# Kernel optimization log

Hardware: AMD Instinct MI355X
Metric: run time of the kernel (lower is better)

The kernel has to match this reference:

```python
import jax, jax.numpy as jnp
import numpy as np

B, L, D, N_HEADS = 4, 8192, 1024, 16
HD = D // N_HEADS
MASK_NEG = -1e10


def setup_inputs() -> dict:
    key = jax.random.key(0)
    ks = jax.random.split(key, 5)
    # xavier_normal std for square Dense: sqrt(2/(fan_in+fan_out))
    std = (2.0 / (D + D)) ** 0.5
    return {
        "query": jax.random.normal(ks[0], (B, L, D), dtype=jnp.float32),
        "mask": jax.random.bernoulli(ks[1], 0.1, (B, L)),  # True = masked out
        "Wq": std * jax.random.normal(ks[2], (D, D), dtype=jnp.float32),
        "bq": jnp.zeros((D,), dtype=jnp.float32),
        "Wk": std * jax.random.normal(ks[3], (D, D), dtype=jnp.float32),
        "bk": jnp.zeros((D,), dtype=jnp.float32),
        "Wv": std * jax.random.normal(ks[4], (D, D), dtype=jnp.float32),
        "bv": jnp.zeros((D,), dtype=jnp.float32),
    }


def reference(query, mask, Wq, bq, Wk, bk, Wv, bv):
    # Self-attention: key = value = query (original falls back when key/value are None)
    q = query @ Wq + bq  # [B, L, D]
    k = query @ Wk + bk
    v = query @ Wv + bv
    # split heads: b l (n h) -> b l n h
    qs = q.reshape(B, L, N_HEADS, HD)
    ks_ = k.reshape(B, L, N_HEADS, HD)
    vs = v.reshape(B, L, N_HEADS, HD)
    m = mask[:, :, None, None]  # [B, L, 1, 1], broadcast over heads & dims
    K = jnp.where(m, MASK_NEG, ks_)
    V = jnp.where(m, 0.0, vs)
    # elu kernel feature map: phi(x) = elu(x) + 1 (elu(-1e10)+1 -> 0 for masked keys)
    phiK = jax.nn.elu(K) + 1.0
    phiQ = jax.nn.elu(qs) + 1.0
    # per-head kv summary: [B, N, HD_k, HD_v]
    kv = jnp.einsum('blnk,blnv->bnkv', phiK, V)
    # FAITHFUL to original einsum 'blk,bkv->blk': sums kv over v, elementwise with phiQ
    kv_sum = kv.sum(-1)  # [B, N, HD]
    out = phiQ * kv_sum[:, None, :, :]  # [B, L, N, HD]
    # combine heads: b l n h -> b l (n h)
    return out.reshape(B, L, D)
```

## Files before the change

### kernel.cpp

```cpp
#include <hip/hip_runtime.h>

typedef unsigned short u16;
typedef unsigned int u32;
typedef __attribute__((ext_vector_type(8))) short s16x8;
typedef __attribute__((ext_vector_type(4))) float f32x4;

#define GAS __attribute__((address_space(1)))
#define LAS __attribute__((address_space(3)))

#define BB 4
#define LL 8192
#define DD 1024
#define NH 16
#define HD 64
#define MROWS (BB * LL)
#define NWBT 2064

__device__ __forceinline__ u16 f2bf(float f) {
  u32 u = __builtin_bit_cast(u32, f);
  u32 r = (u + 0x7FFFu + ((u >> 16) & 1u)) >> 16;
  return (u16)r;
}
__device__ __forceinline__ float bf2f(u32 lo) {
  return __builtin_bit_cast(float, lo << 16);
}

__device__ __forceinline__ void async16(const void* g, void* l) {
  __builtin_amdgcn_global_load_lds((const GAS u32*)g, (LAS u32*)l, 16, 0, 0);
}

__device__ __forceinline__ bool get_mask(const void* mp, int row, int mode) {
  if (mode == 2) return ((const unsigned char*)mp)[row] != 0;
  if (mode == 1) return ((const float*)mp)[row] != 0.f;
  return ((const int*)mp)[row] != 0;
}

__global__ void detect_mask(const u32* __restrict__ m, int* __restrict__ flag) {
  int i = blockIdx.x * 256 + threadIdx.x;
  u32 v = m[i];
  int f = 0;
  if (v == 0x3F800000u) f = 1;
  else if (v > 1u) f = 2;
  if (f) atomicMax(flag, f);
}

__global__ void build_wbt(const float* __restrict__ Wq, const float* __restrict__ Wk,
                          u16* __restrict__ WbT) {
  __shared__ float t[32][33];
  const int n0 = blockIdx.x * 32;
  const int k0 = blockIdx.y * 32;
  const float* W = (n0 >> 10) == 0 ? Wq : Wk;
  const int nloc = n0 & 1023;
  const int tx = threadIdx.x, ty = threadIdx.y;
#pragma unroll
  for (int j = 0; j < 32; j += 8)
    t[ty + j][tx] = W[(size_t)(k0 + ty + j) * DD + nloc + tx];
  __syncthreads();
#pragma unroll
  for (int j = 0; j < 32; j += 8)
    WbT[(size_t)(n0 + ty + j) * DD + k0 + tx] = f2bf(t[tx][ty + j]);
}

__global__ void build_wvs(const float* __restrict__ Wv, u16* __restrict__ WbT) {
  int i = blockIdx.x * 256 + threadIdx.x;
  int k = i >> 4, h = i & 15;
  float s = 0.f;
  const float* p = Wv + (size_t)k * DD + h * HD;
#pragma unroll 8
  for (int j = 0; j < 64; ++j) s += p[j];
  WbT[(size_t)(2048 + h) * DD + k] = f2bf(s);
}

__global__ void build_bcat(const float* __restrict__ bq, const float* __restrict__ bk,
                           const float* __restrict__ bv, float* __restrict__ bcat) {
  int i = blockIdx.x * 256 + threadIdx.x;
  if (i < 1024) bcat[i] = bq[i];
  else if (i < 2048) bcat[i] = bk[i - 1024];
  else if (i < 2064) {
    float s = 0.f;
    const float* p = bv + (i - 2048) * HD;
#pragma unroll 8
    for (int j = 0; j < 64; ++j) s += p[j];
    bcat[i] = s;
  }
}

__global__ __launch_bounds__(256) void prep_q(
    const float* __restrict__ query, const u16* __restrict__ WbT,
    const float* __restrict__ bcat, const void* __restrict__ maskp,
    const int* __restrict__ mmode,
    u16* __restrict__ qb, float* __restrict__ sV) {
  __shared__ u16 ldsW[16 * 1024];
  __shared__ u16 ldsA[128 * 64];
  const int tid = threadIdx.x;
  const int lane = tid & 63;
  const int w = tid >> 6;
  const int row0 = blockIdx.x * 128;

  {
    const int h = tid & 15;
    const int cb = tid >> 4;
#pragma unroll
    for (int j = 0; j < 8; ++j) {
      const int c = cb * 8 + j;
      s16x8 v = *(const s16x8*)(WbT + (size_t)(2048 + h) * DD + c * 8);
      *(s16x8*)(ldsW + h * 1024 + (c ^ (h & 7)) * 8) = v;
    }
  }

  const int r_l = tid >> 3;
  const int slot = tid & 7;
  f32x4 acc[2] = {};

  for (int k0 = 0; k0 < DD; k0 += 64) {
    __syncthreads();
#pragma unroll
    for (int i = 0; i < 4; ++i) {
      const int rl = i * 32 + r_l;
      const int seg = slot ^ (rl & 7);
      const float* gp = query + (size_t)(row0 + rl) * DD + k0 + seg * 8;
      float4 v0 = *(const float4*)gp;
      float4 v1 = *(const float4*)(gp + 4);
      s16x8 o;
      o[0] = (short)f2bf(v0.x); o[1] = (short)f2bf(v0.y);
      o[2] = (short)f2bf(v0.z); o[3] = (short)f2bf(v0.w);
      o[4] = (short)f2bf(v1.x); o[5] = (short)f2bf(v1.y);
      o[6] = (short)f2bf(v1.z); o[7] = (short)f2bf(v1.w);
      *(s16x8*)(qb + (size_t)(row0 + rl) * DD + k0 + seg * 8) = o;
      *(s16x8*)(ldsA + rl * 64 + slot * 8) = o;
    }
    __syncthreads();
#pragma unroll
    for (int kk = 0; kk < 2; ++kk) {
      const int segk = kk * 4 + (lane >> 4);
      const int hh = lane & 15;
      const int cc = (k0 >> 3) + segk;
      s16x8 bfr = *(const s16x8*)(ldsW + hh * 1024 + (cc ^ (hh & 7)) * 8);
#pragma unroll
      for (int mi = 0; mi < 2; ++mi) {
        const int r = w * 32 + mi * 16 + hh;
        s16x8 af = *(const s16x8*)(ldsA + r * 64 + ((segk ^ (r & 7))) * 8);
        acc[mi] = __builtin_amdgcn_mfma_f32_16x16x32_bf16(af, bfr, acc[mi], 0, 0, 0);
      }
    }
  }

  const int mode = *mmode;
  const int lanec = lane & 15, laneq = lane >> 4;
#pragma unroll
  for (int mi = 0; mi < 2; ++mi)
#pragma unroll
    for (int r = 0; r < 4; ++r) {
      const int row = row0 + w * 32 + mi * 16 + laneq * 4 + r;
      const bool msk = get_mask(maskp, row, mode);
      float v = acc[mi][r] + bcat[2048 + lanec];
      sV[(size_t)row * NH + lanec] = msk ? 0.f : v;
    }
}

__global__ __launch_bounds__(256) void gemm_qkv(
    const u16* __restrict__ qb, const u16* __restrict__ WbT,
    const float* __restrict__ bcat, const void* __restrict__ maskp,
    const int* __restrict__ mmode,
    const float* __restrict__ sV, float* __restrict__ kv,
    float* __restrict__ out, int phase) {
  __shared__ u16 ldsA[128 * 64];
  __shared__ u16 ldsB[128 * 64];
  const int tid = threadIdx.x;
  const int lane = tid & 63;
  const int w = tid >> 6;
  const int wm = w & 1, wn = w >> 1;
  const int row0 = blockIdx.x * 128;
  const int cy = blockIdx.y;
  const int col0 = phase == 0 ? cy * 128 : 1024 + cy * 128;

  f32x4 acc[4][4] = {};

  const int r_l = tid >> 3;
  const int slot = tid & 7;
  const int seg = slot ^ (r_l & 7);
  const u16* gA = qb + (size_t)(row0 + r_l) * DD + seg * 8;
  const u16* gB = WbT + (size_t)(col0 + r_l) * DD + seg * 8;

  for (int k0 = 0; k0 < DD; k0 += 64) {
    __syncthreads();
#pragma unroll
    for (int i = 0; i < 4; ++i) {
      async16(gA + (size_t)i * 32 * DD + k0, ldsA + (i * 256 + tid) * 8);
      async16(gB + (size_t)i * 32 * DD + k0, ldsB + (i * 256 + tid) * 8);
    }
    __syncthreads();
#pragma unroll
    for (int kk = 0; kk < 2; ++kk) {
      s16x8 af[4], bfr[4];
      const int segk = kk * 4 + (lane >> 4);
#pragma unroll
      for (int mi = 0; mi < 4; ++mi) {
        const int r = wm * 64 + mi * 16 + (lane & 15);
        af[mi] = *(const s16x8*)(ldsA + r * 64 + (segk ^ (r & 7)) * 8);
      }
#pragma unroll
      for (int ni = 0; ni < 4; ++ni) {
        const int r = wn * 64 + ni * 16 + (lane & 15);
        bfr[ni] = *(const s16x8*)(ldsB + r * 64 + (segk ^ (r & 7)) * 8);
      }
#pragma unroll
      for (int mi = 0; mi < 4; ++mi)
#pragma unroll
        for (int ni = 0; ni < 4; ++ni)
          acc[mi][ni] = __builtin_amdgcn_mfma_f32_16x16x32_bf16(af[mi], bfr[ni], acc[mi][ni], 0, 0, 0);
    }
  }

  const int mode = *mmode;
  const int lanec = lane & 15, laneq = lane >> 4;
  const int wcol0 = col0 + wn * 64;
  const int b = row0 >> 13;

  if (phase == 1) {
    const int n = (wcol0 - 1024) >> 6;
    float pc[4] = {0.f, 0.f, 0.f, 0.f};
#pragma unroll
    for (int mi = 0; mi < 4; ++mi) {
#pragma unroll
      for (int r = 0; r < 4; ++r) {
        const int row = row0 + wm * 64 + mi * 16 + laneq * 4 + r;
        const bool msk = get_mask(maskp, row, mode);
        if (!msk) {
          const float sv = sV[(size_t)row * NH + n];
#pragma unroll
          for (int ni = 0; ni < 4; ++ni) {
            const int col = wcol0 + ni * 16 + lanec;
            float v = acc[mi][ni][r] + bcat[col];
            float phi = v > 0.f ? v + 1.f : __expf(v);
            pc[ni] += phi * sv;
          }
        }
      }
    }
#pragma unroll
    for (int ni = 0; ni < 4; ++ni) {
      pc[ni] += __shfl_xor(pc[ni], 16);
      pc[ni] += __shfl_xor(pc[ni], 32);
    }
    if (laneq == 0) {
#pragma unroll
      for (int ni = 0; ni < 4; ++ni) {
        const int colk = wcol0 - 1024 + ni * 16 + lanec;
        atomicAdd(&kv[b * DD + colk], pc[ni]);
      }
    }
  } else {
    float kvv[4];
#pragma unroll
    for (int ni = 0; ni < 4; ++ni)
      kvv[ni] = kv[b * DD + wcol0 + ni * 16 + lanec];
#pragma unroll
    for (int mi = 0; mi < 4; ++mi) {
#pragma unroll
      for (int r = 0; r < 4; ++r) {
        const int row = row0 + wm * 64 + mi * 16 + laneq * 4 + r;
#pragma unroll
        for (int ni = 0; ni < 4; ++ni) {
          const int col = wcol0 + ni * 16 + lanec;
          float v = acc[mi][ni][r] + bcat[col];
          float phi = v > 0.f ? v + 1.f : __expf(v);
          out[(size_t)row * DD + col] = phi * kvv[ni];
        }
      }
    }
  }
}

extern "C" void kernel_launch(void* const* d_in, const int* in_sizes, int n_in,
                              void* d_out, int out_size, void* d_ws, size_t ws_size,
                              hipStream_t stream) {
  const float* query = (const float*)d_in[0];
  const void* maskp = d_in[1];
  const float* Wq = (const float*)d_in[2];
  const float* bq = (const float*)d_in[3];
  const float* Wk = (const float*)d_in[4];
  const float* bk = (const float*)d_in[5];
  const float* Wv = (const float*)d_in[6];
  const float* bv = (const float*)d_in[7];
  float* out = (float*)d_out;

  char* ws = (char*)d_ws;
  u16* qb = (u16*)ws;            ws += (size_t)MROWS * DD * 2;
  u16* WbT = (u16*)ws;           ws += (size_t)NWBT * DD * 2;
  float* sV = (float*)ws;        ws += (size_t)MROWS * NH * 4;
  float* bcat = (float*)ws;      ws += (size_t)NWBT * 4;
  float* kv = (float*)ws;        ws += (size_t)BB * DD * 4;
  int* mflag = (int*)ws;         ws += 256;

  hipMemsetAsync(kv, 0, (size_t)BB * DD * 4 + 256, stream);

  detect_mask<<<32, 256, 0, stream>>>((const u32*)maskp, mflag);
  build_wbt<<<dim3(2048 / 32, DD / 32), dim3(32, 8), 0, stream>>>(Wq, Wk, WbT);
  build_wvs<<<64, 256, 0, stream>>>(Wv, WbT);
  build_bcat<<<(NWBT + 255) / 256, 256, 0, stream>>>(bq, bk, bv, bcat);
  prep_q<<<MROWS / 128, 256, 0, stream>>>(query, WbT, bcat, maskp, mflag, qb, sV);
  gemm_qkv<<<dim3(MROWS / 128, 8), 256, 0, stream>>>(
      qb, WbT, bcat, maskp, mflag, sV, kv, out, 1);
  gemm_qkv<<<dim3(MROWS / 128, 8), 256, 0, stream>>>(
      qb, WbT, bcat, maskp, mflag, sV, kv, out, 0);
}
```

Before: 471.8 us.

## Rewrite QKV GEMM as 256x256 tile, 8-wave double-buffered pipelined kernel

Replaces the 128x128 single-buffered GEMM with 256x256 tiles computed by 8 waves. K-tiles are split into 32-wide halves and double-buffered in 128KB of LDS, with async global loads interleaved between MFMA groups. It uses explicit barriers, vmcnt waits and s_setprio, plus a block-index swizzle for L2 locality. The aim is to hide global load latency and raise MFMA utilisation and data reuse. In exchange it uses large LDS and register footprints and relies on fragile hand-tuned wait counts.

```diff
diff --git a/kernel.cpp b/kernel.cpp
--- a/kernel.cpp
+++ b/kernel.cpp
@@ -158,73 +158,124 @@
     }
 }
 
-__global__ __launch_bounds__(256) void gemm_qkv(
+#define BUFSZ 8192
+#define UOFF(buf, mat, ks) (((((buf)*2 + (mat))*2 + (ks))) * BUFSZ)
+
+__global__ __launch_bounds__(512, 2) void gemm_qkv(
     const u16* __restrict__ qb, const u16* __restrict__ WbT,
     const float* __restrict__ bcat, const void* __restrict__ maskp,
     const int* __restrict__ mmode,
     const float* __restrict__ sV, float* __restrict__ kv,
     float* __restrict__ out, int phase) {
-  __shared__ u16 ldsA[128 * 64];
-  __shared__ u16 ldsB[128 * 64];
+  __shared__ __align__(16) u16 lds[65536];
   const int tid = threadIdx.x;
   const int lane = tid & 63;
   const int w = tid >> 6;
   const int wm = w & 1, wn = w >> 1;
-  const int row0 = blockIdx.x * 128;
-  const int cy = blockIdx.y;
-  const int col0 = phase == 0 ? cy * 128 : 1024 + cy * 128;
-
-  f32x4 acc[4][4] = {};
-
-  const int r_l = tid >> 3;
-  const int slot = tid & 7;
-  const int seg = slot ^ (r_l & 7);
-  const u16* gA = qb + (size_t)(row0 + r_l) * DD + seg * 8;
-  const u16* gB = WbT + (size_t)(col0 + r_l) * DD + seg * 8;
-
-  for (int k0 = 0; k0 < DD; k0 += 64) {
-    __syncthreads();
-#pragma unroll
-    for (int i = 0; i < 4; ++i) {
-      async16(gA + (size_t)i * 32 * DD + k0, ldsA + (i * 256 + tid) * 8);
-      async16(gB + (size_t)i * 32 * DD + k0, ldsB + (i * 256 + tid) * 8);
-    }
-    __syncthreads();
-#pragma unroll
-    for (int kk = 0; kk < 2; ++kk) {
-      s16x8 af[4], bfr[4];
-      const int segk = kk * 4 + (lane >> 4);
-#pragma unroll
-      for (int mi = 0; mi < 4; ++mi) {
-        const int r = wm * 64 + mi * 16 + (lane & 15);
-        af[mi] = *(const s16x8*)(ldsA + r * 64 + (segk ^ (r & 7)) * 8);
-      }
-#pragma unroll
-      for (int ni = 0; ni < 4; ++ni) {
-        const int r = wn * 64 + ni * 16 + (lane & 15);
-        bfr[ni] = *(const s16x8*)(ldsB + r * 64 + (segk ^ (r & 7)) * 8);
-      }
-#pragma unroll
-      for (int mi = 0; mi < 4; ++mi)
-#pragma unroll
-        for (int ni = 0; ni < 4; ++ni)
-          acc[mi][ni] = __builtin_amdgcn_mfma_f32_16x16x32_bf16(af[mi], bfr[ni], acc[mi][ni], 0, 0, 0);
-    }
+  const int l15 = lane & 15, l16 = lane >> 4;
+
+  const int bid = blockIdx.x;
+  const int swz = (bid & 7) * 64 + (bid >> 3);
+  const int mt = swz >> 2;
+  const int nt = swz & 3;
+  const int row0 = mt * 256;
+  const int col0 = (phase ? 1024 : 0) + nt * 256;
+
+  f32x4 acc[8][4] = {};
+
+#define STAGE(buf, mat, ks, kt) do {                                        \
+    const u16* gb_ = (mat) ? (WbT + (size_t)col0 * DD)                      \
+                           : (qb + (size_t)row0 * DD);                      \
+    const int kt_ = (kt) & 15;                                              \
+    _Pragma("unroll")                                                       \
+    for (int j_ = 0; j_ < 2; ++j_) {                                        \
+      int li_ = tid + j_ * 512;                                             \
+      int row_ = li_ >> 2, slot_ = li_ & 3;                                 \
+      int c_ = slot_ ^ ((row_ >> 1) & 3);                                   \
+      async16(gb_ + (size_t)row_ * DD + kt_ * 64 + (ks) * 32 + c_ * 8,      \
+              lds + UOFF(buf, mat, ks) + li_ * 8);                          \
+    }                                                                       \
+  } while (0)
+
+#define LDA(buf, ks, a) do {                                                \
+    _Pragma("unroll")                                                       \
+    for (int mi_ = 0; mi_ < 8; ++mi_) {                                     \
+      int r_ = wm * 128 + mi_ * 16 + l15;                                   \
+      a[mi_] = *(const s16x8*)(lds + UOFF(buf, 0, ks) + r_ * 32 +           \
+                               ((l16 ^ ((r_ >> 1) & 3)) * 8));              \
+    }                                                                       \
+  } while (0)
+
+#define LDB2(buf, ks, nb, b) do {                                           \
+    _Pragma("unroll")                                                       \
+    for (int q_ = 0; q_ < 2; ++q_) {                                        \
+      int r_ = wn * 64 + ((nb)*2 + q_) * 16 + l15;                          \
+      b[q_] = *(const s16x8*)(lds + UOFF(buf, 1, ks) + r_ * 32 +            \
+                              ((l16 ^ ((r_ >> 1) & 3)) * 8));               \
+    }                                                                       \
+  } while (0)
+
+#define MM(a, b, nb) do {                                                   \
+    __builtin_amdgcn_s_setprio(1);                                          \
+    _Pragma("unroll")                                                       \
+    for (int mi_ = 0; mi_ < 8; ++mi_) {                                     \
+      acc[mi_][(nb)*2] = __builtin_amdgcn_mfma_f32_16x16x32_bf16(           \
+          a[mi_], b[0], acc[mi_][(nb)*2], 0, 0, 0);                         \
+      acc[mi_][(nb)*2 + 1] = __builtin_amdgcn_mfma_f32_16x16x32_bf16(       \
+          a[mi_], b[1], acc[mi_][(nb)*2 + 1], 0, 0, 0);                     \
+    }                                                                       \
+    __builtin_amdgcn_s_setprio(0);                                          \
+  } while (0)
+
+#define BAR() __builtin_amdgcn_s_barrier()
+#define VMW6() asm volatile("s_waitcnt vmcnt(6)" ::: "memory")
+
+  STAGE(0, 0, 0, 0); STAGE(0, 1, 0, 0); STAGE(0, 0, 1, 0); STAGE(0, 1, 1, 0);
+  STAGE(1, 0, 0, 1); STAGE(1, 1, 0, 1); STAGE(1, 0, 1, 1);
+  VMW6();
+  BAR();
+
+  for (int t = 0; t < 16; t += 2) {
+    s16x8 a[8], b[2];
+    LDA(0, 0, a); LDB2(0, 0, 0, b);
+    STAGE(1, 1, 1, t + 1);
+    BAR(); MM(a, b, 0); BAR();
+    LDB2(0, 0, 1, b);
+    STAGE(0, 0, 0, t + 2);
+    BAR(); MM(a, b, 1); BAR();
+    LDA(0, 1, a); LDB2(0, 1, 0, b);
+    STAGE(0, 1, 0, t + 2);
+    BAR(); MM(a, b, 0); BAR();
+    LDB2(0, 1, 1, b);
+    STAGE(0, 0, 1, t + 2);
+    BAR(); MM(a, b, 1); VMW6(); BAR();
+    LDA(1, 0, a); LDB2(1, 0, 0, b);
+    STAGE(0, 1, 1, t + 2);
+    BAR(); MM(a, b, 0); BAR();
+    LDB2(1, 0, 1, b);
+    STAGE(1, 0, 0, t + 3);
+    BAR(); MM(a, b, 1); BAR();
+    LDA(1, 1, a); LDB2(1, 1, 0, b);
+    STAGE(1, 1, 0, t + 3);
+    BAR(); MM(a, b, 0); BAR();
+    LDB2(1, 1, 1, b);
+    STAGE(1, 0, 1, t + 3);
+    BAR(); MM(a, b, 1); VMW6(); BAR();
   }
 
   const int mode = *mmode;
   const int lanec = lane & 15, laneq = lane >> 4;
   const int wcol0 = col0 + wn * 64;
-  const int b = row0 >> 13;
+  const int b_ = row0 >> 13;
 
   if (phase == 1) {
     const int n = (wcol0 - 1024) >> 6;
     float pc[4] = {0.f, 0.f, 0.f, 0.f};
 #pragma unroll
-    for (int mi = 0; mi < 4; ++mi) {
+    for (int mi = 0; mi < 8; ++mi) {
 #pragma unroll
       for (int r = 0; r < 4; ++r) {
-        const int row = row0 + wm * 64 + mi * 16 + laneq * 4 + r;
+        const int row = row0 + wm * 128 + mi * 16 + laneq * 4 + r;
         const bool msk = get_mask(maskp, row, mode);
         if (!msk) {
           const float sv = sV[(size_t)row * NH + n];
@@ -247,19 +298,19 @@
 #pragma unroll
       for (int ni = 0; ni < 4; ++ni) {
         const int colk = wcol0 - 1024 + ni * 16 + lanec;
-        atomicAdd(&kv[b * DD + colk], pc[ni]);
+        atomicAdd(&kv[b_ * DD + colk], pc[ni]);
       }
     }
   } else {
     float kvv[4];
 #pragma unroll
     for (int ni = 0; ni < 4; ++ni)
-      kvv[ni] = kv[b * DD + wcol0 + ni * 16 + lanec];
-#pragma unroll
-    for (int mi = 0; mi < 4; ++mi) {
+      kvv[ni] = kv[b_ * DD + wcol0 + ni * 16 + lanec];
+#pragma unroll
+    for (int mi = 0; mi < 8; ++mi) {
 #pragma unroll
       for (int r = 0; r < 4; ++r) {
-        const int row = row0 + wm * 64 + mi * 16 + laneq * 4 + r;
+        const int row = row0 + wm * 128 + mi * 16 + laneq * 4 + r;
 #pragma unroll
         for (int ni = 0; ni < 4; ++ni) {
           const int col = wcol0 + ni * 16 + lanec;
@@ -300,8 +351,6 @@
   build_wvs<<<64, 256, 0, stream>>>(Wv, WbT);
   build_bcat<<<(NWBT + 255) / 256, 256, 0, stream>>>(bq, bk, bv, bcat);
   prep_q<<<MROWS / 128, 256, 0, stream>>>(query, WbT, bcat, maskp, mflag, qb, sV);
-  gemm_qkv<<<dim3(MROWS / 128, 8), 256, 0, stream>>>(
-      qb, WbT, bcat, maskp, mflag, sV, kv, out, 1);
-  gemm_qkv<<<dim3(MROWS / 128, 8), 256, 0, stream>>>(
-      qb, WbT, bcat, maskp, mflag, sV, kv, out, 0);
-}
+  gemm_qkv<<<512, 512, 0, stream>>>(qb, WbT, bcat, maskp, mflag, sV, kv, out, 1);
+  gemm_qkv<<<512, 512, 0, stream>>>(qb, WbT, bcat, maskp, mflag, sV, kv, out, 0);
+}
```

Result: faster. 429.4 us (-9.0%).
